# Performance work log

Measured on AMD Instinct MI355X. Metric: run time of the kernel, lower is better.

The kernel has to match this reference:

```python
import jax, jax.numpy as jnp
from jax import lax
import numpy as np

H = 768          # BERT-base hidden size
NLAB = 2         # labelnum
T = NLAB + 2     # CRF tagset incl START/STOP (NCRF++ convention)
START = NLAB     # index 2
STOP = NLAB + 1  # index 3


def setup_inputs() -> dict:
    key = jax.random.key(0)
    ks = jax.random.split(key, 8)
    B, S1 = 64, 513  # S1 = 1 (CLS) + 512 content tokens
    emb = jax.random.normal(ks[0], (B, S1, H), dtype=jnp.float32)
    answer_seq_label = jax.random.randint(ks[1], (B, S1), 0, NLAB)
    IsQA = jax.random.randint(ks[2], (B,), 0, 2)
    fc2_W = jax.random.normal(ks[3], (2, H), dtype=jnp.float32) * 0.02
    fc2_b = jnp.zeros((2,), dtype=jnp.float32)
    crf_W = jax.random.normal(ks[4], (T, H), dtype=jnp.float32) * 0.02
    crf_b = jnp.zeros((T,), dtype=jnp.float32)
    transitions = jax.random.normal(ks[5], (T, T), dtype=jnp.float32) * 0.1
    return {"emb": emb, "answer_seq_label": answer_seq_label, "IsQA": IsQA,
            "fc2_W": fc2_W, "fc2_b": fc2_b, "crf_W": crf_W, "crf_b": crf_b,
            "transitions": transitions}


def _crf_log_partition(feats, trans):
    # feats [B,S,T]; linear-chain forward algorithm (log-sum-exp scan)
    alpha0 = feats[:, 0] + trans[START][None]           # [B,T]
    def step(alpha, feat_t):
        # alpha[b,prev] + trans[prev,cur] -> logsumexp over prev
        new = jax.nn.logsumexp(alpha[:, :, None] + trans[None], axis=1) + feat_t
        return new, None
    alpha, _ = lax.scan(step, alpha0, jnp.swapaxes(feats[:, 1:], 0, 1))
    return jax.nn.logsumexp(alpha + trans[:, STOP][None], axis=1)  # [B]


def _crf_gold_score(feats, tags, trans):
    # feats [B,S,T], tags [B,S]
    emit = jnp.take_along_axis(feats, tags[:, :, None], axis=2)[..., 0].sum(axis=1)
    tr = trans[tags[:, :-1], tags[:, 1:]].sum(axis=1)
    tr = tr + trans[START, tags[:, 0]] + trans[tags[:, -1], STOP]
    return emit + tr


def _crf_viterbi(feats, trans):
    # feats [B,S,T] -> best path [B,S]
    delta0 = feats[:, 0] + trans[START][None]
    def step(delta, feat_t):
        scores = delta[:, :, None] + trans[None]   # [B,prev,cur]
        bp = jnp.argmax(scores, axis=1)            # [B,T]
        return jnp.max(scores, axis=1) + feat_t, bp
    delta, bps = lax.scan(step, delta0, jnp.swapaxes(feats[:, 1:], 0, 1))  # bps [S-1,B,T]
    last_tag = jnp.argmax(delta + trans[:, STOP][None], axis=1)            # [B]
    def back(tag, bp_t):
        prev = jnp.take_along_axis(bp_t, tag[:, None], axis=1)[:, 0]
        return prev, prev
    _, path_prefix = lax.scan(back, last_tag, bps, reverse=True)           # [S-1,B]
    return jnp.concatenate([path_prefix, last_tag[None]], axis=0).T        # [B,S]


def reference(emb, answer_seq_label, IsQA, fc2_W, fc2_b, crf_W, crf_b, transitions):
    # CLS head + cross-entropy
    cls_emb = emb[:, 0]                              # [B,H]
    isqa_logits = cls_emb @ fc2_W.T + fc2_b          # [B,2]
    logp = jax.nn.log_softmax(isqa_logits, axis=-1)
    isqa_loss = -jnp.take_along_axis(logp, IsQA[:, None], axis=1).mean()
    isqa_pred = jnp.argmax(isqa_logits, axis=-1)[:, None]
    # CRF head (dropout = identity in eval); feats [B,S,T]
    feats = jnp.einsum('bsh,th->bst', emb[:, 1:], crf_W) + crf_b
    tags = answer_seq_label[:, 1:]
    Z = _crf_log_partition(feats, transitions)
    gold = _crf_gold_score(feats, tags, transitions)
    crf_loss = jnp.mean(Z - gold)
    crf_pred = _crf_viterbi(feats, transitions)
    return (isqa_pred, crf_pred, isqa_loss, crf_loss, tags, IsQA[:, None])
```

## Files before the change

kernel.cpp:

```cpp
#include <hip/hip_runtime.h>
#include <math.h>

#define B     64
#define S1    513
#define S     512
#define H     768
#define T     4
#define START 2
#define STOP  3

#define OUT_ISQA_PRED 0
#define OUT_CRF_PRED  64
#define OUT_ISQA_LOSS 32832
#define OUT_CRF_LOSS  32833
#define OUT_TAGS      32834
#define OUT_ISQA      65602

#define WS_FEATS  0
#define WS_LOGITS (B*S*T)
#define WS_ZG     (B*S*T + 2*B)
#define WS_CNT    (B*S*T + 3*B)

template<int CTRL>
__device__ __forceinline__ float dppf(float x) {
    int v = __builtin_amdgcn_update_dpp(__builtin_bit_cast(int, x),
                                        __builtin_bit_cast(int, x),
                                        CTRL, 0xF, 0xF, false);
    return __builtin_bit_cast(float, v);
}

__device__ __forceinline__ float lse4(float x0, float x1, float x2, float x3) {
    float m = fmaxf(fmaxf(x0, x1), fmaxf(x2, x3));
    return m + __logf(__expf(x0 - m) + __expf(x1 - m) +
                      __expf(x2 - m) + __expf(x3 - m));
}

__global__ __launch_bounds__(256, 6) void feats_kernel(
    const float* __restrict__ emb,
    const float* __restrict__ fc2_W, const float* __restrict__ fc2_b,
    const float* __restrict__ crf_W, const float* __restrict__ crf_b,
    float* __restrict__ ws)
{
    __shared__ float wlds[6 * H];
    for (int i = threadIdx.x; i < 6 * H; i += 256)
        wlds[i] = (i < 4 * H) ? crf_W[i] : fc2_W[i - 4 * H];
    if (blockIdx.x == 0 && threadIdx.x == 0)
        ((int*)ws)[WS_CNT] = 0;
    __syncthreads();

    const int tid  = threadIdx.x;
    const int lane = tid & 63;
    const int l16  = lane & 15;
    const int gw   = blockIdx.x * 4 + (tid >> 6);
    const int r    = gw * 4 + (lane >> 4);
    const int b    = r / S1;
    const int s    = r - b * S1;

    const float4* __restrict__ row4 = (const float4*)emb + (size_t)r * (H / 4);
    const float4* __restrict__ wl4  = (const float4*)wlds;
    const int o0 = s ? 0 * 192 : 4 * 192;
    const int o1 = s ? 1 * 192 : 5 * 192;
    const int o2 = s ? 2 * 192 : 4 * 192;
    const int o3 = s ? 3 * 192 : 5 * 192;

    float a0 = 0.f, a1 = 0.f, a2 = 0.f, a3 = 0.f;
    #pragma unroll 4
    for (int k = 0; k < 12; ++k) {
        const int idx = l16 + 16 * k;
        float4 e  = row4[idx];
        float4 w0 = wl4[o0 + idx];
        float4 w1 = wl4[o1 + idx];
        float4 w2 = wl4[o2 + idx];
        float4 w3 = wl4[o3 + idx];
        a0 += e.x * w0.x + e.y * w0.y + e.z * w0.z + e.w * w0.w;
        a1 += e.x * w1.x + e.y * w1.y + e.z * w1.z + e.w * w1.w;
        a2 += e.x * w2.x + e.y * w2.y + e.z * w2.z + e.w * w2.w;
        a3 += e.x * w3.x + e.y * w3.y + e.z * w3.z + e.w * w3.w;
    }
    a0 += dppf<0xB1>(a0); a0 += dppf<0x4E>(a0);
    a1 += dppf<0xB1>(a1); a1 += dppf<0x4E>(a1);
    a2 += dppf<0xB1>(a2); a2 += dppf<0x4E>(a2);
    a3 += dppf<0xB1>(a3); a3 += dppf<0x4E>(a3);
    a0 += __shfl_xor(a0, 4); a0 += __shfl_xor(a0, 8);
    a1 += __shfl_xor(a1, 4); a1 += __shfl_xor(a1, 8);
    a2 += __shfl_xor(a2, 4); a2 += __shfl_xor(a2, 8);
    a3 += __shfl_xor(a3, 4); a3 += __shfl_xor(a3, 8);

    if (l16 == 0) {
        if (s) {
            float4 o;
            o.x = a0 + crf_b[0]; o.y = a1 + crf_b[1];
            o.z = a2 + crf_b[2]; o.w = a3 + crf_b[3];
            ((float4*)(ws + WS_FEATS))[b * S + (s - 1)] = o;
        } else {
            ws[WS_LOGITS + 2 * b + 0] = a0 + fc2_b[0];
            ws[WS_LOGITS + 2 * b + 1] = a1 + fc2_b[1];
        }
    }
}

__global__ __launch_bounds__(256) void crf_kernel(
    const int* __restrict__ ans, const int* __restrict__ isqa,
    const float* __restrict__ trans,
    float* __restrict__ ws, float* __restrict__ out)
{
    __shared__ float smemf[10240];
    __shared__ int isLast;
    const int tid = threadIdx.x;
    const int blk = blockIdx.x;

    if (blk < 64) {
        const int b = blk;
        float* sf  = smemf;
        float* C   = smemf + 2048;
        float* red = smemf + 3072;

        float tr[16];
        #pragma unroll
        for (int i = 0; i < 16; ++i) tr[i] = trans[i];

        {
            float4* sf4 = (float4*)sf;
            const float4* src4 = (const float4*)(ws + WS_FEATS) + b * 512;
            sf4[tid] = src4[tid];
            sf4[tid + 256] = src4[tid + 256];
        }
        __syncthreads();

        float g = 0.f;
        #pragma unroll
        for (int u = 0; u < 2; ++u) {
            const int t   = 2 * tid + u;
            const int tag = ans[b * S1 + 1 + t];
            out[OUT_TAGS + b * S + t] = (float)tag;
            g += sf[t * 4 + tag];
            g += (t == 0) ? tr[START * 4 + tag] : tr[ans[b * S1 + t] * 4 + tag];
            if (t == S - 1) g += tr[tag * 4 + STOP];
        }
        #pragma unroll
        for (int m = 32; m; m >>= 1) g += __shfl_xor(g, m);
        if ((tid & 63) == 0) red[tid >> 6] = g;

        const int c  = tid >> 2;
        const int jr = tid & 3;
        const int t0 = c ? 8 * c : 1;
        float rl[4];
        #pragma unroll
        for (int i = 0; i < 4; ++i) rl[i] = tr[jr * 4 + i] + sf[t0 * 4 + i];
        for (int t = t0 + 1; t <= 8 * c + 7; ++t) {
            const float f0 = sf[t*4+0], f1 = sf[t*4+1], f2 = sf[t*4+2], f3 = sf[t*4+3];
            float nr[4];
            #pragma unroll
            for (int i = 0; i < 4; ++i)
                nr[i] = lse4(rl[0] + tr[0*4+i], rl[1] + tr[1*4+i],
                             rl[2] + tr[2*4+i], rl[3] + tr[3*4+i]);
            rl[0] = nr[0] + f0; rl[1] = nr[1] + f1;
            rl[2] = nr[2] + f2; rl[3] = nr[3] + f3;
        }
        ((float4*)C)[c * 4 + jr] = make_float4(rl[0], rl[1], rl[2], rl[3]);
        __syncthreads();

        for (int d = 1; d <= 32; d <<= 1) {
            const int cs = (c >= d) ? (c - d) : c;
            float4 ar = ((float4*)C)[cs * 4 + jr];
            float4 b0 = ((float4*)C)[c * 4 + 0];
            float4 b1 = ((float4*)C)[c * 4 + 1];
            float4 b2 = ((float4*)C)[c * 4 + 2];
            float4 b3 = ((float4*)C)[c * 4 + 3];
            __syncthreads();
            if (c >= d) {
                float4 nr;
                nr.x = lse4(ar.x + b0.x, ar.y + b1.x, ar.z + b2.x, ar.w + b3.x);
                nr.y = lse4(ar.x + b0.y, ar.y + b1.y, ar.z + b2.y, ar.w + b3.y);
                nr.z = lse4(ar.x + b0.z, ar.y + b1.z, ar.z + b2.z, ar.w + b3.z);
                nr.w = lse4(ar.x + b0.w, ar.y + b1.w, ar.z + b2.w, ar.w + b3.w);
                ((float4*)C)[c * 4 + jr] = nr;
            }
            __syncthreads();
        }

        if (tid == 0) {
            const float gold = red[0] + red[1] + red[2] + red[3];
            float a0k[4];
            #pragma unroll
            for (int k = 0; k < 4; ++k) a0k[k] = sf[k] + tr[START * 4 + k];
            const float* P = C + 63 * 16;
            float aN[4];
            #pragma unroll
            for (int i = 0; i < 4; ++i)
                aN[i] = lse4(a0k[0] + P[0*4+i], a0k[1] + P[1*4+i],
                             a0k[2] + P[2*4+i], a0k[3] + P[3*4+i]);
            const float Z = lse4(aN[0] + tr[0*4+STOP], aN[1] + tr[1*4+STOP],
                                 aN[2] + tr[2*4+STOP], aN[3] + tr[3*4+STOP]);
            ws[WS_ZG + b] = Z - gold;
            out[OUT_ISQA + b] = (float)isqa[b];
            __threadfence();
            const int old = atomicAdd((int*)ws + WS_CNT, 1);
            isLast = (old == 63);
        }
        __syncthreads();

        if (isLast && tid < 64) {
            __threadfence();
            const float zg = ws[WS_ZG + tid];
            const float l0 = ws[WS_LOGITS + tid * 2 + 0];
            const float l1 = ws[WS_LOGITS + tid * 2 + 1];
            const float m  = fmaxf(l0, l1);
            const float lse = m + __logf(__expf(l0 - m) + __expf(l1 - m));
            const int   y   = isqa[tid];
            const float li  = lse - (y ? l1 : l0);
            float s1 = zg, s2 = li;
            #pragma unroll
            for (int d = 32; d; d >>= 1) {
                s1 += __shfl_xor(s1, d);
                s2 += __shfl_xor(s2, d);
            }
            out[OUT_ISQA_PRED + tid] = (l1 > l0) ? 1.0f : 0.0f;
            if (tid == 0) {
                out[OUT_CRF_LOSS]  = s1 * (1.0f / 64.0f);
                out[OUT_ISQA_LOSS] = s2 * (1.0f / 64.0f);
            }
        }
    } else {
        const int bv = blk - 64;
        float* sfw = smemf;
        unsigned int* bpw = (unsigned int*)(smemf + 8192);
        {
            float4* d4 = (float4*)sfw;
            const float4* s4 = (const float4*)(ws + WS_FEATS) + bv * 4 * 512;
            #pragma unroll
            for (int n = 0; n < 8; ++n) d4[tid + 256 * n] = s4[tid + 256 * n];
        }
        if (tid < 4) bpw[tid * 512] = 0x03020100u;
        __syncthreads();

        const int w    = tid >> 6;
        const int lane = tid & 63;
        const int j    = lane & 3;
        const int b    = bv * 4 + w;
        const float* myf = sfw + w * 2048;
        unsigned char* mybp = (unsigned char*)(bpw + w * 512);

        const float tc0 = trans[0*4+j], tc1 = trans[1*4+j];
        const float tc2 = trans[2*4+j], tc3 = trans[3*4+j];
        const float tjs = trans[j*4 + STOP];

        float d = myf[j] + trans[START * 4 + j];
        float fcur = myf[4 + j];
        for (int t = 1; t < 512; ++t) {
            const float fnext = myf[(t + 1) * 4 + j];
            const float d0 = dppf<0x00>(d), d1 = dppf<0x55>(d);
            const float d2 = dppf<0xAA>(d), d3 = dppf<0xFF>(d);
            const float y0 = d0 + tc0, y1 = d1 + tc1;
            const float y2 = d2 + tc2, y3 = d3 + tc3;
            float bv01 = y0; int bi01 = 0;
            if (y1 > bv01) { bv01 = y1; bi01 = 1; }
            float bv23 = y2; int bi23 = 2;
            if (y3 > bv23) { bv23 = y3; bi23 = 3; }
            float bvv = bv01; int bi = bi01;
            if (bv23 > bvv) { bvv = bv23; bi = bi23; }
            d = bvv + fcur;
            fcur = fnext;
            if (lane < 4) mybp[t * 4 + j] = (unsigned char)bi;
        }

        const float vj = d + tjs;
        const float z0 = dppf<0x00>(vj), z1 = dppf<0x55>(vj);
        const float z2 = dppf<0xAA>(vj), z3 = dppf<0xFF>(vj);
        float m01 = z0; unsigned int i01 = 0;
        if (z1 > m01) { m01 = z1; i01 = 1; }
        float m23 = z2; unsigned int i23 = 2;
        if (z3 > m23) { m23 = z3; i23 = 3; }
        const unsigned int lt = (m23 > m01) ? i23 : i01;

        __syncthreads();

        const uint4 wv0 = ((const uint4*)(bpw + w * 512))[lane * 2 + 0];
        const uint4 wv1 = ((const uint4*)(bpw + w * 512))[lane * 2 + 1];
        unsigned int wk[8] = {wv0.x, wv0.y, wv0.z, wv0.w, wv1.x, wv1.y, wv1.z, wv1.w};
        unsigned int G = wk[7];
        #pragma unroll
        for (int k = 6; k >= 0; --k)
            G = __builtin_amdgcn_perm(0u, wk[k], G);
        unsigned int Sm = G;
        #pragma unroll
        for (int dd = 1; dd < 64; dd <<= 1) {
            const int srcl = lane + dd;
            const unsigned int oth = __shfl(Sm, (srcl < 64) ? srcl : 63);
            if (srcl < 64) Sm = __builtin_amdgcn_perm(0u, Sm, oth);
        }
        unsigned int emap = __shfl(Sm, (lane < 63) ? lane + 1 : 63);
        if (lane == 63) emap = 0x03020100u;
        unsigned int cur = (emap >> (8 * lt)) & 3u;

        float tg[8];
        tg[7] = (float)cur;
        #pragma unroll
        for (int k = 7; k >= 1; --k) {
            cur = (wk[k] >> (8 * cur)) & 3u;
            tg[k - 1] = (float)cur;
        }
        float4* op = (float4*)(out + OUT_CRF_PRED + b * S + lane * 8);
        op[0] = make_float4(tg[0], tg[1], tg[2], tg[3]);
        op[1] = make_float4(tg[4], tg[5], tg[6], tg[7]);
    }
}

extern "C" void kernel_launch(void* const* d_in, const int* in_sizes, int n_in,
                              void* d_out, int out_size, void* d_ws, size_t ws_size,
                              hipStream_t stream)
{
    const float* emb    = (const float*)d_in[0];
    const int*   ans    = (const int*)d_in[1];
    const int*   isqa   = (const int*)d_in[2];
    const float* fc2_W  = (const float*)d_in[3];
    const float* fc2_b  = (const float*)d_in[4];
    const float* crf_W  = (const float*)d_in[5];
    const float* crf_b  = (const float*)d_in[6];
    const float* trans  = (const float*)d_in[7];
    float* out = (float*)d_out;
    float* ws  = (float*)d_ws;

    feats_kernel<<<2052, 256, 0, stream>>>(emb, fc2_W, fc2_b, crf_W, crf_b, ws);
    crf_kernel<<<80, 256, 0, stream>>>(ans, isqa, trans, ws, out);
}
```

Measured before the change: 210.4 us.

## Persistent register-weight feats kernel, transposed feats for Viterbi, packed backpointers

The feats kernel now keeps crf_W in registers and runs a persistent grid of 1024 blocks, where each wave processes 8 full rows with whole-wave reductions, replacing the LDS weight staging. The CLS fc2 logits move into the CRF kernel. Feats are also written in a transposed per-tag layout so the Viterbi loop can read float4 vectors of four timesteps. The Viterbi recurrence packs four backpointers into a word via DPP OR-reduction and writes them as uint4, instead of doing per-step byte stores. This adds an extra scattered transposed store in the feats kernel and puts a serial CLS dot product on the CRF critical path.

```diff
diff --git a/kernel.cpp b/kernel.cpp
--- a/kernel.cpp
+++ b/kernel.cpp
@@ -20,6 +20,7 @@
 #define WS_LOGITS (B*S*T)
 #define WS_ZG     (B*S*T + 2*B)
 #define WS_CNT    (B*S*T + 3*B)
+#define WS_FEATST 131280
 
 template<int CTRL>
 __device__ __forceinline__ float dppf(float x) {
@@ -28,6 +29,10 @@
                                         CTRL, 0xF, 0xF, false);
     return __builtin_bit_cast(float, v);
 }
+template<int CTRL>
+__device__ __forceinline__ int dppi(int x) {
+    return __builtin_amdgcn_update_dpp(x, x, CTRL, 0xF, 0xF, false);
+}
 
 __device__ __forceinline__ float lse4(float x0, float x1, float x2, float x3) {
     float m = fmaxf(fmaxf(x0, x1), fmaxf(x2, x3));
@@ -35,76 +40,94 @@
                       __expf(x2 - m) + __expf(x3 - m));
 }
 
-__global__ __launch_bounds__(256, 6) void feats_kernel(
+__device__ __forceinline__ float wred(float a) {
+    a += dppf<0xB1>(a); a += dppf<0x4E>(a);
+    a += __shfl_xor(a, 4); a += __shfl_xor(a, 8);
+    a += __shfl_xor(a, 16); a += __shfl_xor(a, 32);
+    return a;
+}
+
+__global__ __launch_bounds__(256) void feats_kernel(
     const float* __restrict__ emb,
-    const float* __restrict__ fc2_W, const float* __restrict__ fc2_b,
     const float* __restrict__ crf_W, const float* __restrict__ crf_b,
     float* __restrict__ ws)
 {
-    __shared__ float wlds[6 * H];
-    for (int i = threadIdx.x; i < 6 * H; i += 256)
-        wlds[i] = (i < 4 * H) ? crf_W[i] : fc2_W[i - 4 * H];
     if (blockIdx.x == 0 && threadIdx.x == 0)
         ((int*)ws)[WS_CNT] = 0;
-    __syncthreads();
 
     const int tid  = threadIdx.x;
     const int lane = tid & 63;
-    const int l16  = lane & 15;
-    const int gw   = blockIdx.x * 4 + (tid >> 6);
-    const int r    = gw * 4 + (lane >> 4);
-    const int b    = r / S1;
-    const int s    = r - b * S1;
-
-    const float4* __restrict__ row4 = (const float4*)emb + (size_t)r * (H / 4);
-    const float4* __restrict__ wl4  = (const float4*)wlds;
-    const int o0 = s ? 0 * 192 : 4 * 192;
-    const int o1 = s ? 1 * 192 : 5 * 192;
-    const int o2 = s ? 2 * 192 : 4 * 192;
-    const int o3 = s ? 3 * 192 : 5 * 192;
-
-    float a0 = 0.f, a1 = 0.f, a2 = 0.f, a3 = 0.f;
-    #pragma unroll 4
-    for (int k = 0; k < 12; ++k) {
-        const int idx = l16 + 16 * k;
-        float4 e  = row4[idx];
-        float4 w0 = wl4[o0 + idx];
-        float4 w1 = wl4[o1 + idx];
-        float4 w2 = wl4[o2 + idx];
-        float4 w3 = wl4[o3 + idx];
-        a0 += e.x * w0.x + e.y * w0.y + e.z * w0.z + e.w * w0.w;
-        a1 += e.x * w1.x + e.y * w1.y + e.z * w1.z + e.w * w1.w;
-        a2 += e.x * w2.x + e.y * w2.y + e.z * w2.z + e.w * w2.w;
-        a3 += e.x * w3.x + e.y * w3.y + e.z * w3.z + e.w * w3.w;
+    const int wid  = blockIdx.x * 4 + (tid >> 6);
+
+    const float4* __restrict__ W4 = (const float4*)crf_W;
+    float4 wr[4][3];
+    #pragma unroll
+    for (int o = 0; o < 4; ++o)
+        #pragma unroll
+        for (int k = 0; k < 3; ++k)
+            wr[o][k] = W4[o * 192 + lane + 64 * k];
+    const float cb0 = crf_b[0], cb1 = crf_b[1], cb2 = crf_b[2], cb3 = crf_b[3];
+
+    float* __restrict__ fN = ws + WS_FEATS;
+    float* __restrict__ fT = ws + WS_FEATST;
+
+    #pragma unroll
+    for (int i = 0; i < 8; ++i) {
+        const int row = wid + 4096 * i;
+        const int b   = row >> 9;
+        const int s   = (row & 511) + 1;
+        const float4* __restrict__ src4 =
+            (const float4*)emb + (size_t)(b * S1 + s) * (H / 4);
+
+        float a0 = 0.f, a1 = 0.f, a2 = 0.f, a3 = 0.f;
+        #pragma unroll
+        for (int k = 0; k < 3; ++k) {
+            const float4 e = src4[lane + 64 * k];
+            a0 += e.x * wr[0][k].x + e.y * wr[0][k].y + e.z * wr[0][k].z + e.w * wr[0][k].w;
+            a1 += e.x * wr[1][k].x + e.y * wr[1][k].y + e.z * wr[1][k].z + e.w * wr[1][k].w;
+            a2 += e.x * wr[2][k].x + e.y * wr[2][k].y + e.z * wr[2][k].z + e.w * wr[2][k].w;
+            a3 += e.x * wr[3][k].x + e.y * wr[3][k].y + e.z * wr[3][k].z + e.w * wr[3][k].w;
+        }
+        a0 = wred(a0); a1 = wred(a1); a2 = wred(a2); a3 = wred(a3);
+
+        if (lane == 0) {
+            const float v0 = a0 + cb0, v1 = a1 + cb1, v2 = a2 + cb2, v3 = a3 + cb3;
+            ((float4*)fN)[b * S + (s - 1)] = make_float4(v0, v1, v2, v3);
+            const int tb = b * 4 * S + (s - 1);
+            fT[tb + 0 * S] = v0;
+            fT[tb + 1 * S] = v1;
+            fT[tb + 2 * S] = v2;
+            fT[tb + 3 * S] = v3;
+        }
     }
-    a0 += dppf<0xB1>(a0); a0 += dppf<0x4E>(a0);
-    a1 += dppf<0xB1>(a1); a1 += dppf<0x4E>(a1);
-    a2 += dppf<0xB1>(a2); a2 += dppf<0x4E>(a2);
-    a3 += dppf<0xB1>(a3); a3 += dppf<0x4E>(a3);
-    a0 += __shfl_xor(a0, 4); a0 += __shfl_xor(a0, 8);
-    a1 += __shfl_xor(a1, 4); a1 += __shfl_xor(a1, 8);
-    a2 += __shfl_xor(a2, 4); a2 += __shfl_xor(a2, 8);
-    a3 += __shfl_xor(a3, 4); a3 += __shfl_xor(a3, 8);
-
-    if (l16 == 0) {
-        if (s) {
-            float4 o;
-            o.x = a0 + crf_b[0]; o.y = a1 + crf_b[1];
-            o.z = a2 + crf_b[2]; o.w = a3 + crf_b[3];
-            ((float4*)(ws + WS_FEATS))[b * S + (s - 1)] = o;
-        } else {
-            ws[WS_LOGITS + 2 * b + 0] = a0 + fc2_b[0];
-            ws[WS_LOGITS + 2 * b + 1] = a1 + fc2_b[1];
-        }
-    }
+}
+
+__device__ __forceinline__ unsigned int vstep(
+    float& d, float fv,
+    float tc0, float tc1, float tc2, float tc3, int sh8j)
+{
+    const float d0 = dppf<0x00>(d), d1 = dppf<0x55>(d);
+    const float d2 = dppf<0xAA>(d), d3 = dppf<0xFF>(d);
+    const float y0 = d0 + tc0, y1 = d1 + tc1;
+    const float y2 = d2 + tc2, y3 = d3 + tc3;
+    const float m01 = fmaxf(y0, y1), m23 = fmaxf(y2, y3);
+    const int   i01 = (y1 > y0) ? 1 : 0;
+    const int   i23 = (y3 > y2) ? 3 : 2;
+    const int   bi  = (m23 > m01) ? i23 : i01;
+    d = fmaxf(m01, m23) + fv;
+    unsigned int mb = (unsigned int)bi << sh8j;
+    unsigned int t1 = mb | (unsigned int)dppi<0xB1>((int)mb);
+    return t1 | (unsigned int)dppi<0x4E>((int)t1);
 }
 
 __global__ __launch_bounds__(256) void crf_kernel(
     const int* __restrict__ ans, const int* __restrict__ isqa,
+    const float* __restrict__ emb,
+    const float* __restrict__ fc2_W, const float* __restrict__ fc2_b,
     const float* __restrict__ trans,
     float* __restrict__ ws, float* __restrict__ out)
 {
-    __shared__ float smemf[10240];
+    __shared__ float smemf[10784];
     __shared__ int isLast;
     const int tid = threadIdx.x;
     const int blk = blockIdx.x;
@@ -124,6 +147,25 @@
             const float4* src4 = (const float4*)(ws + WS_FEATS) + b * 512;
             sf4[tid] = src4[tid];
             sf4[tid + 256] = src4[tid + 256];
+        }
+
+        if (tid < 128) {
+            const int wv   = tid >> 6;
+            const int lane = tid & 63;
+            const float4* e4 = (const float4*)emb + (size_t)b * S1 * (H / 4);
+            const float4* w4 = (const float4*)fc2_W + wv * 192;
+            float acc = 0.f;
+            #pragma unroll
+            for (int k = 0; k < 3; ++k) {
+                const float4 e = e4[lane + 64 * k];
+                const float4 w = w4[lane + 64 * k];
+                acc += e.x * w.x + e.y * w.y + e.z * w.z + e.w * w.w;
+            }
+            acc = wred(acc);
+            if (lane == 0) {
+                ws[WS_LOGITS + 2 * b + wv] = acc + fc2_b[wv];
+                __threadfence();
+            }
         }
         __syncthreads();
 
@@ -223,45 +265,50 @@
         }
     } else {
         const int bv = blk - 64;
-        float* sfw = smemf;
-        unsigned int* bpw = (unsigned int*)(smemf + 8192);
+        float* sfT = smemf;
+        unsigned int* bpw = (unsigned int*)(smemf + 8208);
         {
-            float4* d4 = (float4*)sfw;
-            const float4* s4 = (const float4*)(ws + WS_FEATS) + bv * 4 * 512;
+            float4* d4 = (float4*)sfT;
+            const float4* s4 = (const float4*)(ws + WS_FEATST) + bv * 4 * 512;
             #pragma unroll
             for (int n = 0; n < 8; ++n) d4[tid + 256 * n] = s4[tid + 256 * n];
         }
-        if (tid < 4) bpw[tid * 512] = 0x03020100u;
+        if (tid < 4) ((float4*)(sfT + 8192))[tid & 3] =
+            make_float4(0.f, 0.f, 0.f, 0.f);
         __syncthreads();
 
         const int w    = tid >> 6;
         const int lane = tid & 63;
         const int j    = lane & 3;
         const int b    = bv * 4 + w;
-        const float* myf = sfw + w * 2048;
-        unsigned char* mybp = (unsigned char*)(bpw + w * 512);
+        const int sh8j = 8 * j;
 
         const float tc0 = trans[0*4+j], tc1 = trans[1*4+j];
         const float tc2 = trans[2*4+j], tc3 = trans[3*4+j];
+        const float tSj = trans[START*4+j];
         const float tjs = trans[j*4 + STOP];
 
-        float d = myf[j] + trans[START * 4 + j];
-        float fcur = myf[4 + j];
-        for (int t = 1; t < 512; ++t) {
-            const float fnext = myf[(t + 1) * 4 + j];
-            const float d0 = dppf<0x00>(d), d1 = dppf<0x55>(d);
-            const float d2 = dppf<0xAA>(d), d3 = dppf<0xFF>(d);
-            const float y0 = d0 + tc0, y1 = d1 + tc1;
-            const float y2 = d2 + tc2, y3 = d3 + tc3;
-            float bv01 = y0; int bi01 = 0;
-            if (y1 > bv01) { bv01 = y1; bi01 = 1; }
-            float bv23 = y2; int bi23 = 2;
-            if (y3 > bv23) { bv23 = y3; bi23 = 3; }
-            float bvv = bv01; int bi = bi01;
-            if (bv23 > bvv) { bvv = bv23; bi = bi23; }
-            d = bvv + fcur;
-            fcur = fnext;
-            if (lane < 4) mybp[t * 4 + j] = (unsigned char)bi;
+        const float4* colT4 = (const float4*)(sfT + w * 2048 + j * 512);
+        uint4* bpq = (uint4*)(bpw + w * 512);
+
+        float4 A  = colT4[0];
+        float4 Bq = colT4[1];
+        float4 B2 = colT4[2];
+        float d = A.x + tSj;
+        {
+            const unsigned int W1 = vstep(d, A.y, tc0, tc1, tc2, tc3, sh8j);
+            const unsigned int W2 = vstep(d, A.z, tc0, tc1, tc2, tc3, sh8j);
+            const unsigned int W3 = vstep(d, A.w, tc0, tc1, tc2, tc3, sh8j);
+            if (lane == 0) bpq[0] = make_uint4(0x03020100u, W1, W2, W3);
+        }
+        for (int g = 1; g < 128; ++g) {
+            const float4 Cq = colT4[g + 2];
+            const unsigned int W0 = vstep(d, Bq.x, tc0, tc1, tc2, tc3, sh8j);
+            const unsigned int W1 = vstep(d, Bq.y, tc0, tc1, tc2, tc3, sh8j);
+            const unsigned int W2 = vstep(d, Bq.z, tc0, tc1, tc2, tc3, sh8j);
+            const unsigned int W3 = vstep(d, Bq.w, tc0, tc1, tc2, tc3, sh8j);
+            if (lane == 0) bpq[g] = make_uint4(W0, W1, W2, W3);
+            Bq = B2; B2 = Cq;
         }
 
         const float vj = d + tjs;
@@ -275,8 +322,8 @@
 
         __syncthreads();
 
-        const uint4 wv0 = ((const uint4*)(bpw + w * 512))[lane * 2 + 0];
-        const uint4 wv1 = ((const uint4*)(bpw + w * 512))[lane * 2 + 1];
+        const uint4 wv0 = bpq[lane * 2 + 0];
+        const uint4 wv1 = bpq[lane * 2 + 1];
         unsigned int wk[8] = {wv0.x, wv0.y, wv0.z, wv0.w, wv1.x, wv1.y, wv1.z, wv1.w};
         unsigned int G = wk[7];
         #pragma unroll
@@ -321,6 +368,6 @@
     float* out = (float*)d_out;
     float* ws  = (float*)d_ws;
 
-    feats_kernel<<<2052, 256, 0, stream>>>(emb, fc2_W, fc2_b, crf_W, crf_b, ws);
-    crf_kernel<<<80, 256, 0, stream>>>(ans, isqa, trans, ws, out);
-}
+    feats_kernel<<<1024, 256, 0, stream>>>(emb, crf_W, crf_b, ws);
+    crf_kernel<<<80, 256, 0, stream>>>(ans, isqa, emb, fc2_W, fc2_b, trans, ws, out);
+}
```

New measurement: 195.1 us. -7.3%, faster.
